# Kernel optimization log

Hardware: AMD Instinct MI355X
Metric: run time of the kernel (lower is better)

## Reference

```python
import jax, jax.numpy as jnp
import numpy as np

N, E, F_IN, H, C = 100000, 1250000, 512, 64, 40
K = 2


def _lin_w(key, fan_out, fan_in):
    bound = 1.0 / np.sqrt(fan_in)
    return jax.random.uniform(key, (fan_out, fan_in), jnp.float32, -bound, bound)


def setup_inputs() -> dict:
    key = jax.random.key(0)
    ks = jax.random.split(key, 14)
    x = jax.random.normal(ks[0], (N, F_IN), dtype=jnp.float32)
    edge_index = jax.random.randint(ks[1], (2, E), 0, N, dtype=jnp.int64)
    inp = {
        "x": x,
        "edge_index": edge_index,
        "W_in": _lin_w(ks[2], H, F_IN),
        "b_in": jnp.zeros((H,), jnp.float32),
        "W1_0": _lin_w(ks[3], H, H),
        "W2_0": _lin_w(ks[4], H, H),
        "Wf_0": _lin_w(ks[5], H, H),
        "W1_1": _lin_w(ks[6], H, H),
        "W2_1": _lin_w(ks[7], H, H),
        "Wf_1": _lin_w(ks[8], H, H),
        "W_out": _lin_w(ks[9], C, H),
        "b_out": jnp.zeros((C,), jnp.float32),
    }
    return inp


def _step_conv(Q, row, col, W1, W2, Wf, n):
    # StepConv.forward with step == 0 (the only valid branch in the source)
    h3 = Q @ W1.T              # [N, H]
    h4 = Q @ W2.T              # [N, H]
    hloop = jax.nn.relu(Q @ Wf.T)
    # edge gate: s = sigmoid(-<h3[row], h4[col]>)  per edge
    s = jax.nn.sigmoid(-jnp.sum(h3[row] * h4[col], axis=1))  # [E]
    # propagate (source_to_target): scatter messages from row into col
    agg3 = jax.ops.segment_sum(s[:, None] * h3[row], col, num_segments=n)
    agg4 = jax.ops.segment_sum((1.0 - s)[:, None] * h4[row], col, num_segments=n)
    return hloop + agg3 - agg4


def reference(x, edge_index, W_in, b_in, W1_0, W2_0, Wf_0, W1_1, W2_1, Wf_1, W_out, b_out):
    n = x.shape[0]
    row, col = edge_index[0], edge_index[1]
    Q = x @ W_in.T + b_in
    for (W1, W2, Wf) in ((W1_0, W2_0, Wf_0), (W1_1, W2_1, Wf_1)):
        hq3 = _step_conv(Q, row, col, W1, W2, Wf, n)
        # F.normalize(p=2, dim=1), eps=1e-12
        Q = hq3 / jnp.maximum(jnp.linalg.norm(hq3, axis=1, keepdims=True), 1e-12)
    logits = Q @ W_out.T + b_out
    return jax.nn.log_softmax(logits, axis=1)
```

## Files before the change

### kernel.cpp

```cpp
#include <hip/hip_runtime.h>
#include <hip/hip_bf16.h>
#include <math.h>

#define H 64
#define FIN 512
#define COUT 40

typedef __attribute__((ext_vector_type(8))) short bf16x8;
typedef __attribute__((ext_vector_type(4))) float f32x4;

__device__ __forceinline__ unsigned short f2bf(float f) {
    union { float f; unsigned u; } v; v.f = f;
    unsigned r = v.u + 0x7FFF + ((v.u >> 16) & 1);
    return (unsigned short)(r >> 16);
}
__device__ __forceinline__ float bflo(unsigned u) { return __uint_as_float(u << 16); }
__device__ __forceinline__ float bfhi(unsigned u) { return __uint_as_float(u & 0xffff0000u); }

__global__ void k_pack(const float* __restrict__ W_in,
                       const float* __restrict__ W1_0, const float* __restrict__ W2_0,
                       const float* __restrict__ Wf_0,
                       const float* __restrict__ W1_1, const float* __restrict__ W2_1,
                       const float* __restrict__ Wf_1,
                       uint4* __restrict__ Bp, uint4* __restrict__ Bc0, uint4* __restrict__ Bc1) {
    int t = blockIdx.x * blockDim.x + threadIdx.x;
    const float* src;
    uint4* dst;
    if (t < 4096) {
        int kb = t >> 6, n = t & 63;
        src = &W_in[n * FIN + kb * 8];
        dst = &Bp[t];
    } else if (t < 4096 + 1536) {
        int u = t - 4096;
        int j = u >> 9, kb = (u >> 6) & 7, n = u & 63;
        const float* W = (j == 0) ? W1_0 : (j == 1) ? W2_0 : Wf_0;
        src = &W[n * H + kb * 8];
        dst = &Bc0[u];
    } else if (t < 4096 + 3072) {
        int u = t - 4096 - 1536;
        int j = u >> 9, kb = (u >> 6) & 7, n = u & 63;
        const float* W = (j == 0) ? W1_1 : (j == 1) ? W2_1 : Wf_1;
        src = &W[n * H + kb * 8];
        dst = &Bc1[u];
    } else return;
    float4 a0 = *(const float4*)&src[0];
    float4 a1 = *(const float4*)&src[4];
    uint4 u;
    u.x = ((unsigned)f2bf(a0.y) << 16) | f2bf(a0.x);
    u.y = ((unsigned)f2bf(a0.w) << 16) | f2bf(a0.z);
    u.z = ((unsigned)f2bf(a1.y) << 16) | f2bf(a1.x);
    u.w = ((unsigned)f2bf(a1.w) << 16) | f2bf(a1.z);
    *dst = u;
}

__global__ void k_zero(int* __restrict__ p, int n) {
    int i = blockIdx.x * blockDim.x + threadIdx.x;
    if (i < n) p[i] = 0;
}

__global__ void k_hist(const int* __restrict__ ei, int* __restrict__ deg, int nE) {
    int e = blockIdx.x * blockDim.x + threadIdx.x;
    if (e < nE) atomicAdd(&deg[ei[nE + e]], 1);
}

__global__ __launch_bounds__(256) void k_scan1(const int* __restrict__ deg, int* __restrict__ epos,
                                               int* __restrict__ blocksum, int n) {
    __shared__ int tmp[256];
    int t = threadIdx.x;
    int base = blockIdx.x * 1024 + t * 4;
    int v[4]; int s = 0;
#pragma unroll
    for (int i = 0; i < 4; ++i) { v[i] = (base + i < n) ? deg[base + i] : 0; s += v[i]; }
    tmp[t] = s;
    __syncthreads();
    int incl = s;
    for (int off = 1; off < 256; off <<= 1) {
        int y = (t >= off) ? tmp[t - off] : 0;
        __syncthreads();
        incl += y;
        tmp[t] = incl;
        __syncthreads();
    }
    if (t == 255) blocksum[blockIdx.x] = incl;
    int run = incl - s;
#pragma unroll
    for (int i = 0; i < 4; ++i) { if (base + i < n) epos[base + i] = run; run += v[i]; }
}

__global__ __launch_bounds__(256) void k_scan2(const int* __restrict__ blocksum,
                                               int* __restrict__ blockoff, int nb) {
    __shared__ int tmp[256];
    int t = threadIdx.x;
    int s = (t < nb) ? blocksum[t] : 0;
    tmp[t] = s;
    __syncthreads();
    int incl = s;
    for (int off = 1; off < 256; off <<= 1) {
        int y = (t >= off) ? tmp[t - off] : 0;
        __syncthreads();
        incl += y;
        tmp[t] = incl;
        __syncthreads();
    }
    if (t < nb) blockoff[t] = incl - s;
}

__global__ __launch_bounds__(256) void k_scan3(int* __restrict__ epos, const int* __restrict__ blockoff,
                                               int* __restrict__ cursor, int n, int nE) {
    int b = blockIdx.x;
    int off = blockoff[b];
    int base = b * 1024 + threadIdx.x * 4;
#pragma unroll
    for (int i = 0; i < 4; ++i) {
        if (base + i < n) {
            int p = epos[base + i] + off;
            epos[base + i] = p;
            cursor[base + i] = p;
        }
    }
    if (b == 0 && threadIdx.x == 0) epos[n] = nE;
}

__global__ void k_scatter(const int* __restrict__ ei, int* __restrict__ cursor,
                          int* __restrict__ srcidx, int nE) {
    int e = blockIdx.x * blockDim.x + threadIdx.x;
    if (e < nE) {
        int c = ei[nE + e];
        int p = atomicAdd(&cursor[c], 1);
        srcidx[p] = ei[e];
    }
}

__global__ __launch_bounds__(256) void k_in_gemm(
    const float* __restrict__ x, const uint4* __restrict__ Bp,
    const float* __restrict__ bias, unsigned short* __restrict__ qbf, int n) {
    __shared__ uint4 As4[256];
    __shared__ uint4 Bs4[256];
    int tid = threadIdx.x;
    int base = blockIdx.x * 64;
    int lane = tid & 63, w = tid >> 6;

    int srow = tid >> 2;
    int sg = tid & 3;
    int sgs = sg ^ ((srow >> 1) & 3);
    bool rowok = (base + srow) < n;
    const float* xsrc = &x[(size_t)(base + srow) * FIN + sg * 8];

    int arow = 16 * w + (lane & 15);
    int ag = (lane >> 4) ^ ((arow >> 1) & 3);
    int aidx = arow * 4 + ag;
    int kg = lane >> 4;

    f32x4 acc[4];
#pragma unroll
    for (int i = 0; i < 4; ++i) acc[i] = (f32x4){0.f, 0.f, 0.f, 0.f};

    for (int kk = 0; kk < FIN; kk += 32) {
        float4 a0 = make_float4(0.f, 0.f, 0.f, 0.f), a1 = a0;
        if (rowok) {
            a0 = *(const float4*)&xsrc[kk];
            a1 = *(const float4*)&xsrc[kk + 4];
        }
        uint4 bstage = Bp[((kk >> 3) + (tid >> 6)) * 64 + (tid & 63)];
        __syncthreads();
        {
            uint4 u;
            u.x = ((unsigned)f2bf(a0.y) << 16) | f2bf(a0.x);
            u.y = ((unsigned)f2bf(a0.w) << 16) | f2bf(a0.z);
            u.z = ((unsigned)f2bf(a1.y) << 16) | f2bf(a1.x);
            u.w = ((unsigned)f2bf(a1.w) << 16) | f2bf(a1.z);
            As4[srow * 4 + sgs] = u;
            Bs4[tid] = bstage;
        }
        __syncthreads();
        bf16x8 af = *(const bf16x8*)&As4[aidx];
#pragma unroll
        for (int nt = 0; nt < 4; ++nt) {
            bf16x8 bfr = *(const bf16x8*)&Bs4[kg * 64 + nt * 16 + (lane & 15)];
            acc[nt] = __builtin_amdgcn_mfma_f32_16x16x32_bf16(af, bfr, acc[nt], 0, 0, 0);
        }
    }
    int col0 = lane & 15, rowg = lane >> 4;
#pragma unroll
    for (int nt = 0; nt < 4; ++nt) {
        float bv = bias[nt * 16 + col0];
#pragma unroll
        for (int reg = 0; reg < 4; ++reg) {
            int r = base + 16 * w + rowg * 4 + reg;
            if (r < n) qbf[(size_t)r * H + nt * 16 + col0] = f2bf(acc[nt][reg] + bv);
        }
    }
}

__global__ __launch_bounds__(256) void k_layer_gemm(
    const uint4* __restrict__ Qbf, const uint4* __restrict__ Bc,
    unsigned* __restrict__ P, unsigned short* __restrict__ hl, int n) {
    __shared__ uint4 Qs[512];
    int tid = threadIdx.x;
    int base = blockIdx.x * 64;
    int lane = tid & 63, w = tid >> 6;
    {
        int r = tid >> 2, g0 = (tid & 3) * 2;
        uint4 u0 = make_uint4(0u, 0u, 0u, 0u), u1 = u0;
        if (base + r < n) {
            u0 = Qbf[(size_t)(base + r) * 8 + g0];
            u1 = Qbf[(size_t)(base + r) * 8 + g0 + 1];
        }
        Qs[r * 8 + (g0 ^ (r & 7))] = u0;
        Qs[r * 8 + ((g0 + 1) ^ (r & 7))] = u1;
    }
    __syncthreads();

    int arow = w * 16 + (lane & 15);
    f32x4 acc[12];
#pragma unroll
    for (int i = 0; i < 12; ++i) acc[i] = (f32x4){0.f, 0.f, 0.f, 0.f};

#pragma unroll
    for (int ks = 0; ks < 2; ++ks) {
        int g = ks * 4 + (lane >> 4);
        bf16x8 af = *(const bf16x8*)&Qs[arow * 8 + (g ^ (arow & 7))];
#pragma unroll
        for (int j = 0; j < 3; ++j) {
#pragma unroll
            for (int nt = 0; nt < 4; ++nt) {
                bf16x8 bfr = *(const bf16x8*)&Bc[(j * 8 + g) * 64 + nt * 16 + (lane & 15)];
                acc[j * 4 + nt] = __builtin_amdgcn_mfma_f32_16x16x32_bf16(af, bfr, acc[j * 4 + nt], 0, 0, 0);
            }
        }
    }
    int col0 = lane & 15, rowg = lane >> 4;
#pragma unroll
    for (int nt = 0; nt < 4; ++nt) {
#pragma unroll
        for (int reg = 0; reg < 4; ++reg) {
            int r = base + w * 16 + rowg * 4 + reg;
            if (r < n) {
                int col = nt * 16 + col0;
                unsigned pv = ((unsigned)f2bf(acc[4 + nt][reg]) << 16) | f2bf(acc[nt][reg]);
                P[(size_t)r * H + col] = pv;
                hl[(size_t)r * H + col] = f2bf(fmaxf(acc[8 + nt][reg], 0.f));
            }
        }
    }
}

template <int LAYER>
__global__ __launch_bounds__(256) void k_agg(
    const int* __restrict__ rowptr, const int* __restrict__ srcidx,
    const unsigned* __restrict__ P, const unsigned* __restrict__ hl32,
    unsigned* __restrict__ Qbf32,
    const float* __restrict__ W_out, const float* __restrict__ b_out,
    float* __restrict__ out, int n) {
    __shared__ float Wt[H][COUT + 1];
    __shared__ float qrow[4][H];
    int tid = threadIdx.x;
    int lane = tid & 63;
    int w = tid >> 6;
    if (LAYER == 1) {
        for (int idx = tid; idx < H * COUT; idx += 256) {
            int c = idx >> 6, k = idx & 63;
            Wt[k][c] = W_out[idx];
        }
        __syncthreads();
    }
    int c = blockIdx.x * 4 + w;
    if (c >= n) return;
    int q = lane >> 4;
    int j = lane & 15;
    const uint4* P4 = (const uint4*)P;

    uint4 pc = P4[(size_t)c * 16 + j];
    float4 h4c = make_float4(bfhi(pc.x), bfhi(pc.y), bfhi(pc.z), bfhi(pc.w));
    float4 acc = make_float4(0.f, 0.f, 0.f, 0.f);

    int k0 = rowptr[c], k1 = rowptr[c + 1];
    if (k0 < k1) {
        const uint4 Z = make_uint4(0u, 0u, 0u, 0u);
        int e0 = k0 + 2 * q;
        uint4 pA0 = Z, pA1 = Z;
        if (e0 < k1)     pA0 = P4[(size_t)srcidx[e0] * 16 + j];
        if (e0 + 1 < k1) pA1 = P4[(size_t)srcidx[e0 + 1] * 16 + j];

        for (int kb = k0; kb < k1; kb += 8) {
            uint4 pB0 = Z, pB1 = Z;
            int f0 = kb + 8 + 2 * q;
            if (f0 < k1)     pB0 = P4[(size_t)srcidx[f0] * 16 + j];
            if (f0 + 1 < k1) pB1 = P4[(size_t)srcidx[f0 + 1] * 16 + j];

            float4 h30 = make_float4(bflo(pA0.x), bflo(pA0.y), bflo(pA0.z), bflo(pA0.w));
            float4 h40 = make_float4(bfhi(pA0.x), bfhi(pA0.y), bfhi(pA0.z), bfhi(pA0.w));
            float4 h31 = make_float4(bflo(pA1.x), bflo(pA1.y), bflo(pA1.z), bflo(pA1.w));
            float4 h41 = make_float4(bfhi(pA1.x), bfhi(pA1.y), bfhi(pA1.z), bfhi(pA1.w));
            float d0 = h30.x * h4c.x + h30.y * h4c.y + h30.z * h4c.z + h30.w * h4c.w;
            float d1 = h31.x * h4c.x + h31.y * h4c.y + h31.z * h4c.z + h31.w * h4c.w;
            d0 += __shfl_xor(d0, 1, 64);  d1 += __shfl_xor(d1, 1, 64);
            d0 += __shfl_xor(d0, 2, 64);  d1 += __shfl_xor(d1, 2, 64);
            d0 += __shfl_xor(d0, 4, 64);  d1 += __shfl_xor(d1, 4, 64);
            d0 += __shfl_xor(d0, 8, 64);  d1 += __shfl_xor(d1, 8, 64);
            float s0 = 1.0f / (1.0f + __expf(d0));
            float s1 = 1.0f / (1.0f + __expf(d1));
            float t0 = 1.0f - s0, t1 = 1.0f - s1;
            acc.x += s0 * h30.x - t0 * h40.x + s1 * h31.x - t1 * h41.x;
            acc.y += s0 * h30.y - t0 * h40.y + s1 * h31.y - t1 * h41.y;
            acc.z += s0 * h30.z - t0 * h40.z + s1 * h31.z - t1 * h41.z;
            acc.w += s0 * h30.w - t0 * h40.w + s1 * h31.w - t1 * h41.w;
            pA0 = pB0; pA1 = pB1;
        }
    }
    acc.x += __shfl_xor(acc.x, 16, 64);
    acc.y += __shfl_xor(acc.y, 16, 64);
    acc.z += __shfl_xor(acc.z, 16, 64);
    acc.w += __shfl_xor(acc.w, 16, 64);
    acc.x += __shfl_xor(acc.x, 32, 64);
    acc.y += __shfl_xor(acc.y, 32, 64);
    acc.z += __shfl_xor(acc.z, 32, 64);
    acc.w += __shfl_xor(acc.w, 32, 64);

    uint2 hv = *(const uint2*)&hl32[(size_t)c * 32 + j * 2];
    acc.x += bflo(hv.x); acc.y += bfhi(hv.x);
    acc.z += bflo(hv.y); acc.w += bfhi(hv.y);

    float ss = acc.x * acc.x + acc.y * acc.y + acc.z * acc.z + acc.w * acc.w;
    ss += __shfl_xor(ss, 1, 64);
    ss += __shfl_xor(ss, 2, 64);
    ss += __shfl_xor(ss, 4, 64);
    ss += __shfl_xor(ss, 8, 64);
    float inv = 1.0f / fmaxf(sqrtf(ss), 1e-12f);

    if (LAYER == 0) {
        if (lane < 16) {
            uint2 o;
            o.x = ((unsigned)f2bf(acc.y * inv) << 16) | f2bf(acc.x * inv);
            o.y = ((unsigned)f2bf(acc.w * inv) << 16) | f2bf(acc.z * inv);
            *(uint2*)&Qbf32[(size_t)c * 32 + j * 2] = o;
        }
    } else {
        if (lane < 16) {
            float4 o;
            o.x = acc.x * inv; o.y = acc.y * inv; o.z = acc.z * inv; o.w = acc.w * inv;
            *(float4*)&qrow[w][j * 4] = o;
        }
        float logit = -3.0e38f;
        if (lane < COUT) {
            float a = b_out[lane];
#pragma unroll 8
            for (int k = 0; k < H; ++k) a += qrow[w][k] * Wt[k][lane];
            logit = a;
        }
        float m = logit;
#pragma unroll
        for (int off = 32; off; off >>= 1) m = fmaxf(m, __shfl_xor(m, off, 64));
        float ex = (lane < COUT) ? __expf(logit - m) : 0.f;
#pragma unroll
        for (int off = 32; off; off >>= 1) ex += __shfl_xor(ex, off, 64);
        if (lane < COUT) out[(size_t)c * COUT + lane] = (logit - m) - logf(ex);
    }
}

extern "C" void kernel_launch(void* const* d_in, const int* in_sizes, int n_in,
                              void* d_out, int out_size, void* d_ws, size_t ws_size,
                              hipStream_t stream) {
    const float* x     = (const float*)d_in[0];
    const int*   ei    = (const int*)d_in[1];
    const float* W_in  = (const float*)d_in[2];
    const float* b_in  = (const float*)d_in[3];
    const float* W1_0  = (const float*)d_in[4];
    const float* W2_0  = (const float*)d_in[5];
    const float* Wf_0  = (const float*)d_in[6];
    const float* W1_1  = (const float*)d_in[7];
    const float* W2_1  = (const float*)d_in[8];
    const float* Wf_1  = (const float*)d_in[9];
    const float* W_out = (const float*)d_in[10];
    const float* b_out = (const float*)d_in[11];
    float* out = (float*)d_out;

    int N = in_sizes[0] / FIN;
    int E = in_sizes[1] / 2;

    uint4* Bp    = (uint4*)d_ws;
    uint4* Bc0   = Bp + 4096;
    uint4* Bc1   = Bc0 + 1536;
    unsigned* Qbf32 = (unsigned*)(Bc1 + 1536);
    unsigned* P  = Qbf32 + (size_t)N * 32;
    unsigned* hl32 = P + (size_t)N * H;
    int* rowptr  = (int*)(hl32 + (size_t)N * 32);
    int* deg     = rowptr + (N + 2);
    int* cursor  = deg + N;
    int* srcidx  = cursor + N;
    int* blocksum = srcidx + E;
    int* blockoff = blocksum + 256;

    k_pack<<<28, 256, 0, stream>>>(W_in, W1_0, W2_0, Wf_0, W1_1, W2_1, Wf_1, Bp, Bc0, Bc1);

    int nb = (N + 1023) / 1024;
    k_zero<<<(N + 255) / 256, 256, 0, stream>>>(deg, N);
    k_hist<<<(E + 255) / 256, 256, 0, stream>>>(ei, deg, E);
    k_scan1<<<nb, 256, 0, stream>>>(deg, rowptr, blocksum, N);
    k_scan2<<<1, 256, 0, stream>>>(blocksum, blockoff, nb);
    k_scan3<<<nb, 256, 0, stream>>>(rowptr, blockoff, cursor, N, E);
    k_scatter<<<(E + 255) / 256, 256, 0, stream>>>(ei, cursor, srcidx, E);

    int gm = (N + 63) / 64;
    k_in_gemm<<<gm, 256, 0, stream>>>(x, Bp, b_in, (unsigned short*)Qbf32, N);

    int ga = (N + 3) / 4;
    k_layer_gemm<<<gm, 256, 0, stream>>>((const uint4*)Qbf32, Bc0, P, (unsigned short*)hl32, N);
    k_agg<0><<<ga, 256, 0, stream>>>(rowptr, srcidx, P, hl32, Qbf32, W_out, b_out, out, N);
    k_layer_gemm<<<gm, 256, 0, stream>>>((const uint4*)Qbf32, Bc1, P, (unsigned short*)hl32, N);
    k_agg<1><<<ga, 256, 0, stream>>>(rowptr, srcidx, P, hl32, Qbf32, W_out, b_out, out, N);
}
```

Baseline: 407.4 us.

## Split output head into MFMA kernel and restructure edge gather pipeline

```diff
diff --git a/kernel.cpp b/kernel.cpp
--- a/kernel.cpp
+++ b/kernel.cpp
@@ -22,7 +22,9 @@
                        const float* __restrict__ Wf_0,
                        const float* __restrict__ W1_1, const float* __restrict__ W2_1,
                        const float* __restrict__ Wf_1,
-                       uint4* __restrict__ Bp, uint4* __restrict__ Bc0, uint4* __restrict__ Bc1) {
+                       const float* __restrict__ W_out,
+                       uint4* __restrict__ Bp, uint4* __restrict__ Bc0,
+                       uint4* __restrict__ Bc1, uint4* __restrict__ Bo) {
     int t = blockIdx.x * blockDim.x + threadIdx.x;
     const float* src;
     uint4* dst;
@@ -42,6 +44,12 @@
         const float* W = (j == 0) ? W1_1 : (j == 1) ? W2_1 : Wf_1;
         src = &W[n * H + kb * 8];
         dst = &Bc1[u];
+    } else if (t < 4096 + 3072 + 512) {
+        int u = t - 4096 - 3072;
+        int kb = u >> 6, col = u & 63;
+        if (col >= COUT) { Bo[u] = make_uint4(0u, 0u, 0u, 0u); return; }
+        src = &W_out[col * H + kb * 8];
+        dst = &Bo[u];
     } else return;
     float4 a0 = *(const float4*)&src[0];
     float4 a1 = *(const float4*)&src[4];
@@ -245,25 +253,13 @@
     }
 }
 
-template <int LAYER>
 __global__ __launch_bounds__(256) void k_agg(
     const int* __restrict__ rowptr, const int* __restrict__ srcidx,
     const unsigned* __restrict__ P, const unsigned* __restrict__ hl32,
-    unsigned* __restrict__ Qbf32,
-    const float* __restrict__ W_out, const float* __restrict__ b_out,
-    float* __restrict__ out, int n) {
-    __shared__ float Wt[H][COUT + 1];
-    __shared__ float qrow[4][H];
+    unsigned* __restrict__ Qbf32, int n) {
     int tid = threadIdx.x;
     int lane = tid & 63;
     int w = tid >> 6;
-    if (LAYER == 1) {
-        for (int idx = tid; idx < H * COUT; idx += 256) {
-            int c = idx >> 6, k = idx & 63;
-            Wt[k][c] = W_out[idx];
-        }
-        __syncthreads();
-    }
     int c = blockIdx.x * 4 + w;
     if (c >= n) return;
     int q = lane >> 4;
@@ -277,35 +273,35 @@
     int k0 = rowptr[c], k1 = rowptr[c + 1];
     if (k0 < k1) {
         const uint4 Z = make_uint4(0u, 0u, 0u, 0u);
-        int e0 = k0 + 2 * q;
-        uint4 pA0 = Z, pA1 = Z;
-        if (e0 < k1)     pA0 = P4[(size_t)srcidx[e0] * 16 + j];
-        if (e0 + 1 < k1) pA1 = P4[(size_t)srcidx[e0 + 1] * 16 + j];
-
-        for (int kb = k0; kb < k1; kb += 8) {
-            uint4 pB0 = Z, pB1 = Z;
-            int f0 = kb + 8 + 2 * q;
-            if (f0 < k1)     pB0 = P4[(size_t)srcidx[f0] * 16 + j];
-            if (f0 + 1 < k1) pB1 = P4[(size_t)srcidx[f0 + 1] * 16 + j];
-
-            float4 h30 = make_float4(bflo(pA0.x), bflo(pA0.y), bflo(pA0.z), bflo(pA0.w));
-            float4 h40 = make_float4(bfhi(pA0.x), bfhi(pA0.y), bfhi(pA0.z), bfhi(pA0.w));
-            float4 h31 = make_float4(bflo(pA1.x), bflo(pA1.y), bflo(pA1.z), bflo(pA1.w));
-            float4 h41 = make_float4(bfhi(pA1.x), bfhi(pA1.y), bfhi(pA1.z), bfhi(pA1.w));
-            float d0 = h30.x * h4c.x + h30.y * h4c.y + h30.z * h4c.z + h30.w * h4c.w;
-            float d1 = h31.x * h4c.x + h31.y * h4c.y + h31.z * h4c.z + h31.w * h4c.w;
-            d0 += __shfl_xor(d0, 1, 64);  d1 += __shfl_xor(d1, 1, 64);
-            d0 += __shfl_xor(d0, 2, 64);  d1 += __shfl_xor(d1, 2, 64);
-            d0 += __shfl_xor(d0, 4, 64);  d1 += __shfl_xor(d1, 4, 64);
-            d0 += __shfl_xor(d0, 8, 64);  d1 += __shfl_xor(d1, 8, 64);
-            float s0 = 1.0f / (1.0f + __expf(d0));
-            float s1 = 1.0f / (1.0f + __expf(d1));
-            float t0 = 1.0f - s0, t1 = 1.0f - s1;
-            acc.x += s0 * h30.x - t0 * h40.x + s1 * h31.x - t1 * h41.x;
-            acc.y += s0 * h30.y - t0 * h40.y + s1 * h31.y - t1 * h41.y;
-            acc.z += s0 * h30.z - t0 * h40.z + s1 * h31.z - t1 * h41.z;
-            acc.w += s0 * h30.w - t0 * h40.w + s1 * h31.w - t1 * h41.w;
-            pA0 = pB0; pA1 = pB1;
+        int last = k1 - 1;
+        int e0 = k0 + q;
+        int sA = srcidx[min(e0, last)];
+        bool vA = e0 < k1;
+        int sB = srcidx[min(e0 + 4, last)];
+        bool vB = (e0 + 4) < k1;
+        uint4 pA = P4[(size_t)sA * 16 + j];
+        if (!vA) pA = Z;
+
+        for (int kb = k0; kb < k1; kb += 4) {
+            int e2 = kb + 8 + q;
+            int sC = srcidx[min(e2, last)];
+            bool vC = e2 < k1;
+            uint4 pB = P4[(size_t)sB * 16 + j];
+            if (!vB) pB = Z;
+            float4 h3r = make_float4(bflo(pA.x), bflo(pA.y), bflo(pA.z), bflo(pA.w));
+            float4 h4r = make_float4(bfhi(pA.x), bfhi(pA.y), bfhi(pA.z), bfhi(pA.w));
+            float d = h3r.x * h4c.x + h3r.y * h4c.y + h3r.z * h4c.z + h3r.w * h4c.w;
+            d += __shfl_xor(d, 1, 64);
+            d += __shfl_xor(d, 2, 64);
+            d += __shfl_xor(d, 4, 64);
+            d += __shfl_xor(d, 8, 64);
+            float s = 1.0f / (1.0f + __expf(d));
+            float t = 1.0f - s;
+            acc.x += s * h3r.x - t * h4r.x;
+            acc.y += s * h3r.y - t * h4r.y;
+            acc.z += s * h3r.z - t * h4r.z;
+            acc.w += s * h3r.w - t * h4r.w;
+            pA = pB; sB = sC; vB = vC;
         }
     }
     acc.x += __shfl_xor(acc.x, 16, 64);
@@ -328,33 +324,73 @@
     ss += __shfl_xor(ss, 8, 64);
     float inv = 1.0f / fmaxf(sqrtf(ss), 1e-12f);
 
-    if (LAYER == 0) {
-        if (lane < 16) {
-            uint2 o;
-            o.x = ((unsigned)f2bf(acc.y * inv) << 16) | f2bf(acc.x * inv);
-            o.y = ((unsigned)f2bf(acc.w * inv) << 16) | f2bf(acc.z * inv);
-            *(uint2*)&Qbf32[(size_t)c * 32 + j * 2] = o;
-        }
-    } else {
-        if (lane < 16) {
-            float4 o;
-            o.x = acc.x * inv; o.y = acc.y * inv; o.z = acc.z * inv; o.w = acc.w * inv;
-            *(float4*)&qrow[w][j * 4] = o;
-        }
-        float logit = -3.0e38f;
-        if (lane < COUT) {
-            float a = b_out[lane];
-#pragma unroll 8
-            for (int k = 0; k < H; ++k) a += qrow[w][k] * Wt[k][lane];
-            logit = a;
-        }
-        float m = logit;
-#pragma unroll
-        for (int off = 32; off; off >>= 1) m = fmaxf(m, __shfl_xor(m, off, 64));
-        float ex = (lane < COUT) ? __expf(logit - m) : 0.f;
-#pragma unroll
-        for (int off = 32; off; off >>= 1) ex += __shfl_xor(ex, off, 64);
-        if (lane < COUT) out[(size_t)c * COUT + lane] = (logit - m) - logf(ex);
+    if (lane < 16) {
+        uint2 o;
+        o.x = ((unsigned)f2bf(acc.y * inv) << 16) | f2bf(acc.x * inv);
+        o.y = ((unsigned)f2bf(acc.w * inv) << 16) | f2bf(acc.z * inv);
+        *(uint2*)&Qbf32[(size_t)c * 32 + j * 2] = o;
+    }
+}
+
+__global__ __launch_bounds__(256) void k_head(
+    const uint4* __restrict__ Qbf, const uint4* __restrict__ Bo,
+    const float* __restrict__ b_out, float* __restrict__ out, int n) {
+    __shared__ uint4 Qs[512];
+    int tid = threadIdx.x;
+    int base = blockIdx.x * 64;
+    int lane = tid & 63, w = tid >> 6;
+    {
+        int r = tid >> 2, g0 = (tid & 3) * 2;
+        uint4 u0 = make_uint4(0u, 0u, 0u, 0u), u1 = u0;
+        if (base + r < n) {
+            u0 = Qbf[(size_t)(base + r) * 8 + g0];
+            u1 = Qbf[(size_t)(base + r) * 8 + g0 + 1];
+        }
+        Qs[r * 8 + (g0 ^ (r & 7))] = u0;
+        Qs[r * 8 + ((g0 + 1) ^ (r & 7))] = u1;
+    }
+    __syncthreads();
+
+    int arow = w * 16 + (lane & 15);
+    f32x4 acc[3];
+#pragma unroll
+    for (int i = 0; i < 3; ++i) acc[i] = (f32x4){0.f, 0.f, 0.f, 0.f};
+#pragma unroll
+    for (int ks = 0; ks < 2; ++ks) {
+        int g = ks * 4 + (lane >> 4);
+        bf16x8 af = *(const bf16x8*)&Qs[arow * 8 + (g ^ (arow & 7))];
+#pragma unroll
+        for (int nt = 0; nt < 3; ++nt) {
+            bf16x8 bfr = *(const bf16x8*)&Bo[g * 64 + nt * 16 + (lane & 15)];
+            acc[nt] = __builtin_amdgcn_mfma_f32_16x16x32_bf16(af, bfr, acc[nt], 0, 0, 0);
+        }
+    }
+    int col = lane & 15, rowg = lane >> 4;
+    float bv0 = b_out[col];
+    float bv1 = b_out[16 + col];
+    float bv2 = (col < 8) ? b_out[32 + col] : 0.f;
+#pragma unroll
+    for (int reg = 0; reg < 4; ++reg) {
+        int r = base + w * 16 + rowg * 4 + reg;
+        float v0 = acc[0][reg] + bv0;
+        float v1 = acc[1][reg] + bv1;
+        float v2 = (col < 8) ? (acc[2][reg] + bv2) : -3.0e38f;
+        float m = fmaxf(fmaxf(v0, v1), v2);
+        m = fmaxf(m, __shfl_xor(m, 1, 64));
+        m = fmaxf(m, __shfl_xor(m, 2, 64));
+        m = fmaxf(m, __shfl_xor(m, 4, 64));
+        m = fmaxf(m, __shfl_xor(m, 8, 64));
+        float ex = __expf(v0 - m) + __expf(v1 - m) + ((col < 8) ? __expf(v2 - m) : 0.f);
+        ex += __shfl_xor(ex, 1, 64);
+        ex += __shfl_xor(ex, 2, 64);
+        ex += __shfl_xor(ex, 4, 64);
+        ex += __shfl_xor(ex, 8, 64);
+        float lse = m + logf(ex);
+        if (r < n) {
+            out[(size_t)r * COUT + col] = v0 - lse;
+            out[(size_t)r * COUT + 16 + col] = v1 - lse;
+            if (col < 8) out[(size_t)r * COUT + 32 + col] = v2 - lse;
+        }
     }
 }
 
@@ -381,7 +417,8 @@
     uint4* Bp    = (uint4*)d_ws;
     uint4* Bc0   = Bp + 4096;
     uint4* Bc1   = Bc0 + 1536;
-    unsigned* Qbf32 = (unsigned*)(Bc1 + 1536);
+    uint4* Bo    = Bc1 + 1536;
+    unsigned* Qbf32 = (unsigned*)(Bo + 512);
     unsigned* P  = Qbf32 + (size_t)N * 32;
     unsigned* hl32 = P + (size_t)N * H;
     int* rowptr  = (int*)(hl32 + (size_t)N * 32);
@@ -391,7 +428,8 @@
     int* blocksum = srcidx + E;
     int* blockoff = blocksum + 256;
 
-    k_pack<<<28, 256, 0, stream>>>(W_in, W1_0, W2_0, Wf_0, W1_1, W2_1, Wf_1, Bp, Bc0, Bc1);
+    k_pack<<<30, 256, 0, stream>>>(W_in, W1_0, W2_0, Wf_0, W1_1, W2_1, Wf_1, W_out,
+                                   Bp, Bc0, Bc1, Bo);
 
     int nb = (N + 1023) / 1024;
     k_zero<<<(N + 255) / 256, 256, 0, stream>>>(deg, N);
@@ -406,7 +444,8 @@
 
     int ga = (N + 3) / 4;
     k_layer_gemm<<<gm, 256, 0, stream>>>((const uint4*)Qbf32, Bc0, P, (unsigned short*)hl32, N);
-    k_agg<0><<<ga, 256, 0, stream>>>(rowptr, srcidx, P, hl32, Qbf32, W_out, b_out, out, N);
+    k_agg<<<ga, 256, 0, stream>>>(rowptr, srcidx, P, hl32, Qbf32, N);
     k_layer_gemm<<<gm, 256, 0, stream>>>((const uint4*)Qbf32, Bc1, P, (unsigned short*)hl32, N);
-    k_agg<1><<<ga, 256, 0, stream>>>(rowptr, srcidx, P, hl32, Qbf32, W_out, b_out, out, N);
-}
+    k_agg<<<ga, 256, 0, stream>>>(rowptr, srcidx, P, hl32, Qbf32, N);
+    k_head<<<gm, 256, 0, stream>>>((const uint4*)Qbf32, Bo, b_out, out, N);
+}
```

Result: faster. 352.6 us (-13.4%).
